# Performance work log

Hardware: AMD Instinct MI355X
Metric: run time of the kernel (lower is better)

The kernel has to match this reference:

```python
import jax, jax.numpy as jnp
import numpy as np

N_EMBD = 1024
N_HEAD = 16
HEAD_DIM = N_EMBD // N_HEAD


def setup_inputs() -> dict:
    key = jax.random.key(0)
    ks = jax.random.split(key, 5)
    B, S = 2, 2048
    scale = 0.02
    return {
        "hidden_states": jax.random.normal(ks[0], (B, S, N_EMBD), dtype=jnp.float32),
        "w_attn": jax.random.normal(ks[1], (N_EMBD, 3 * N_EMBD), dtype=jnp.float32) * scale,
        "b_attn": jnp.zeros((3 * N_EMBD,), dtype=jnp.float32),
        "w_proj": jax.random.normal(ks[2], (N_EMBD, N_EMBD), dtype=jnp.float32) * scale,
        "b_proj": jnp.zeros((N_EMBD,), dtype=jnp.float32),
    }


def reference(hidden_states, w_attn, b_attn, w_proj, b_proj):
    B, S, _ = hidden_states.shape
    qkv = hidden_states @ w_attn + b_attn                     # [B,S,3E]
    q, k, v = jnp.split(qkv, 3, axis=-1)                      # each [B,S,E]

    def split_heads(t):  # [B,S,E] -> [B,H,S,D]
        return t.reshape(B, S, N_HEAD, HEAD_DIM).transpose(0, 2, 1, 3)

    q, k, v = split_heads(q), split_heads(k), split_heads(v)

    scores = jnp.einsum("bhqd,bhkd->bhqk", q, k) / np.sqrt(HEAD_DIM).astype(np.float32)
    causal = jnp.tril(jnp.ones((S, S), dtype=bool))
    scores = jnp.where(causal[None, None], scores, jnp.float32(-jnp.inf))
    attn = jax.nn.softmax(scores, axis=-1)                    # [B,H,S,S]
    out = jnp.einsum("bhqk,bhkd->bhqd", attn, v)              # [B,H,S,D]
    out = out.transpose(0, 2, 1, 3).reshape(B, S, N_EMBD)     # merge heads
    out = out @ w_proj + b_proj
    return out
```

## Files before the change

kernel.cpp:

```cpp
#include <hip/hip_runtime.h>
#include <hip/hip_bf16.h>


typedef __attribute__((ext_vector_type(4))) float  float4v;
typedef __attribute__((ext_vector_type(8))) short  short8v;
typedef __attribute__((ext_vector_type(4))) short  short4v;

#define ATT_SCALE 0.18033688011112042f

__device__ __forceinline__ short f2bf(float f) {
  union { float f; unsigned u; } v; v.f = f;
  unsigned r = v.u + 0x7fffu + ((v.u >> 16) & 1u);
  return (short)(r >> 16);
}
__device__ __forceinline__ float bf2f(short s) {
  union { unsigned u; float f; } v; v.u = ((unsigned)(unsigned short)s) << 16;
  return v.f;
}

__device__ __forceinline__ short4v pack_bf16x4(float a, float b, float c, float d) {
  unsigned x0 = __builtin_bit_cast(unsigned, a) + 0x8000u;
  unsigned x1 = __builtin_bit_cast(unsigned, b) + 0x8000u;
  unsigned x2 = __builtin_bit_cast(unsigned, c) + 0x8000u;
  unsigned x3 = __builtin_bit_cast(unsigned, d) + 0x8000u;
  union { unsigned u[2]; short4v s; } r;
  r.u[0] = __builtin_amdgcn_perm(x1, x0, 0x07060302);
  r.u[1] = __builtin_amdgcn_perm(x3, x2, 0x07060302);
  return r.s;
}

__device__ __forceinline__ void gl_lds16(const void* g, void* l) {
  __builtin_amdgcn_global_load_lds(
      (const __attribute__((address_space(1))) unsigned*)g,
      (__attribute__((address_space(3))) unsigned*)l, 16, 0, 0);
}

__global__ __launch_bounds__(256) void prep_kernel(
    const float* __restrict__ hidden, const float* __restrict__ w_attn,
    const float* __restrict__ w_proj, short* __restrict__ hA,
    short* __restrict__ wqkvT, short* __restrict__ wprojT) {
  __shared__ float tile[32][33];
  const int bx = blockIdx.x, t = threadIdx.x;
  if (bx < 4096) {
    const size_t i = ((size_t)bx * 256 + t) * 4;
    float4v v = *(const float4v*)(hidden + i);
    short4v o;
    #pragma unroll
    for (int k = 0; k < 4; k++) o[k] = f2bf(v[k]);
    *(short4v*)(hA + i) = o;
    return;
  }
  const float* in; short* out; int R, C, cx, cy;
  if (bx < 4096 + 3072) {
    in = w_attn; out = wqkvT; R = 1024; C = 3072;
    cx = (bx - 4096) % 96; cy = (bx - 4096) / 96;
  } else {
    in = w_proj; out = wprojT; R = 1024; C = 1024;
    cx = (bx - 7168) % 32; cy = (bx - 7168) / 32;
  }
  const int tx = t & 31, ty = t >> 5;
  const int c0 = cx * 32, r0 = cy * 32;
  #pragma unroll
  for (int i = 0; i < 4; i++)
    tile[ty + i * 8][tx] = in[(size_t)(r0 + ty + i * 8) * C + c0 + tx];
  __syncthreads();
  #pragma unroll
  for (int i = 0; i < 4; i++) {
    const int cc = ty + i * 8;
    out[(size_t)(c0 + cc) * R + r0 + tx] = f2bf(tile[tx][cc]);
  }
}

template<int RB, int MODE>
__global__ __launch_bounds__(256) void gemm_bt(
    const short* __restrict__ A, const short* __restrict__ Bt,
    const float* __restrict__ bias, void* __restrict__ Cout,
    short* __restrict__ vA, int M, int N, int K)
{
  __shared__ short As[RB][32];
  __shared__ short Bs[128][32];
  const int MI = RB / 32;
  const int t    = threadIdx.x;
  const int lane = t & 63;
  const int wave = t >> 6;
  const int wm   = (wave >> 1) * (RB / 2);
  const int wn   = (wave & 1) * 64;
  const int l16  = lane & 15;
  const int quad = lane >> 4;
  const int row0 = blockIdx.y * RB;
  const int col0 = blockIdx.x * 128;

  float4v acc[MI][4] = {};

  const int srow = lane >> 2;
  const int scol = (lane & 3) * 8;

  for (int k0 = 0; k0 < K; k0 += 32) {
    if (RB == 128) {
      #pragma unroll
      for (int h = 0; h < 2; h++)
        gl_lds16(A + (size_t)(row0 + wave * 32 + h * 16 + srow) * K + k0 + scol,
                 &As[(wave * 32 + h * 16 + srow) & (RB - 1)][scol]);
    } else {
      gl_lds16(A + (size_t)(row0 + wave * 16 + srow) * K + k0 + scol,
               &As[(wave * 16 + srow) & (RB - 1)][scol]);
    }
    #pragma unroll
    for (int h = 0; h < 2; h++)
      gl_lds16(Bt + (size_t)(col0 + wave * 32 + h * 16 + srow) * K + k0 + scol,
               &Bs[wave * 32 + h * 16 + srow][scol]);
    __syncthreads();
    short8v af[MI], bf[4];
    #pragma unroll
    for (int i = 0; i < MI; i++)
      af[i] = *(const short8v*)&As[wm + i * 16 + l16][quad * 8];
    #pragma unroll
    for (int j = 0; j < 4; j++)
      bf[j] = *(const short8v*)&Bs[wn + j * 16 + l16][quad * 8];
    #pragma unroll
    for (int i = 0; i < MI; i++)
      #pragma unroll
      for (int j = 0; j < 4; j++)
        acc[i][j] = __builtin_amdgcn_mfma_f32_16x16x32_bf16(af[i], bf[j], acc[i][j], 0, 0, 0);
    __syncthreads();
  }

  if (MODE == 2 && col0 >= 2048) {
    const int b  = row0 >> 11;
    const int hh = ((col0 - 2048) >> 6) + (wn >> 6);
    const int kt = ((row0 & 2047) >> 6) + (wm >> 6);
    short* vbase = vA + ((size_t)((b * 16 + hh) * 32 + kt) * 8) * 512;
    #pragma unroll
    for (int j = 0; j < 4; j++) {
      const float bv = bias[col0 + wn + j * 16 + l16];
      #pragma unroll
      for (int kwp = 0; kwp < 2; kwp++) {
        short8v s8;
        #pragma unroll
        for (int kw = 0; kw < 2; kw++) {
          short4v q4 = pack_bf16x4(acc[kwp * 2 + kw][j][0] + bv,
                                   acc[kwp * 2 + kw][j][1] + bv,
                                   acc[kwp * 2 + kw][j][2] + bv,
                                   acc[kwp * 2 + kw][j][3] + bv);
          #pragma unroll
          for (int r = 0; r < 4; r++) s8[kw * 4 + r] = q4[r];
        }
        *(short8v*)(vbase + ((size_t)(kwp * 4 + j) * 64 + lane) * 8) = s8;
      }
    }
    return;
  }

  #pragma unroll
  for (int j = 0; j < 4; j++) {
    const int col = col0 + wn + j * 16 + l16;
    const float sc = (MODE == 2 && col < 1024) ? ATT_SCALE : 1.0f;
    const float bv = bias[col];
    #pragma unroll
    for (int i = 0; i < MI; i++) {
      #pragma unroll
      for (int r = 0; r < 4; r++) {
        const int row = row0 + wm + i * 16 + quad * 4 + r;
        const float v = (acc[i][j][r] + bv) * sc;
        if (MODE == 2) ((short*)Cout)[(size_t)row * N + col] = f2bf(v);
        else           ((float*)Cout)[(size_t)row * N + col] = v;
      }
    }
  }
}

__global__ __launch_bounds__(256, 2) void attn_mfma(
    const short* __restrict__ qkv, const short* __restrict__ vA,
    short* __restrict__ P0, short* __restrict__ P1, float* __restrict__ lp)
{
  __shared__ short KA[2][8 * 512];
  __shared__ short VA[2][8 * 512];

  const int bh = blockIdx.y;
  const int b = bh >> 4, h = bh & 15;
  const int s = blockIdx.x;
  int qt = 0, sbase = 0;
  for (;;) { const int nc = (qt >> 3) + 1; if (s < sbase + nc) break; sbase += nc; qt++; }
  const int c = s - sbase;
  const int kt0  = c * 8;
  const int kend = min(qt + 1, kt0 + 8);

  const int t = threadIdx.x;
  const int lane = t & 63, w = t >> 6;
  const int l16 = lane & 15, quad = lane >> 4;

  const size_t base = (size_t)b * 2048 * 3072;
  const int qoff = h * 64, koff = 1024 + h * 64;
  const int qg = qt * 64 + w * 16 + l16;

  short8v qf[2];
  #pragma unroll
  for (int ks = 0; ks < 2; ks++)
    qf[ks] = *(const short8v*)(qkv + base + (size_t)qg * 3072 + qoff + ks * 32 + quad * 8);

  float4v O[4] = {};
  float l = 0.0f;

  const int id0 = w * 2, id1 = id0 + 1;
  const int jm0 = id0 & 3, ks0 = id0 >> 2;
  const int jm1 = id1 & 3, ks1 = id1 >> 2;
  const short* kg0 = qkv + base + (size_t)(jm0 * 16 + l16) * 3072 + koff + ks0 * 32 + quad * 8;
  const short* kg1 = qkv + base + (size_t)(jm1 * 16 + l16) * 3072 + koff + ks1 * 32 + quad * 8;
  const short* vg  = vA + (size_t)(bh * 32) * 4096 + lane * 8;

  gl_lds16(kg0 + (size_t)kt0 * 64 * 3072, &KA[0][id0 * 512 + lane * 8]);
  gl_lds16(kg1 + (size_t)kt0 * 64 * 3072, &KA[0][id1 * 512 + lane * 8]);
  gl_lds16(vg + (size_t)kt0 * 4096 + id0 * 512, &VA[0][id0 * 512 + lane * 8]);
  gl_lds16(vg + (size_t)kt0 * 4096 + id1 * 512, &VA[0][id1 * 512 + lane * 8]);

  for (int kt = kt0; kt < kend; kt++) {
    const int buf = (kt - kt0) & 1;
    __syncthreads();
    if (kt + 1 < kend) {
      gl_lds16(kg0 + (size_t)(kt + 1) * 64 * 3072, &KA[buf ^ 1][id0 * 512 + lane * 8]);
      gl_lds16(kg1 + (size_t)(kt + 1) * 64 * 3072, &KA[buf ^ 1][id1 * 512 + lane * 8]);
      gl_lds16(vg + (size_t)(kt + 1) * 4096 + id0 * 512, &VA[buf ^ 1][id0 * 512 + lane * 8]);
      gl_lds16(vg + (size_t)(kt + 1) * 4096 + id1 * 512, &VA[buf ^ 1][id1 * 512 + lane * 8]);
    }

    float4v sv[4] = {};
    #pragma unroll
    for (int ks = 0; ks < 2; ks++)
      #pragma unroll
      for (int jm = 0; jm < 4; jm++) {
        const short8v kf = *(const short8v*)&KA[buf][(ks * 4 + jm) * 512 + lane * 8];
        sv[jm] = __builtin_amdgcn_mfma_f32_16x16x32_bf16(kf, qf[ks], sv[jm], 0, 0, 0);
      }

    if (kt == qt) {
      #pragma unroll
      for (int jm = 0; jm < 4; jm++) {
        const int kv = kt * 64 + jm * 16 + quad * 4;
        #pragma unroll
        for (int r = 0; r < 4; r++)
          if (kv + r > qg) sv[jm][r] = -INFINITY;
      }
    }

    short4v pk[4];
    #pragma unroll
    for (int jm = 0; jm < 4; jm++) {
      float p0 = exp2f(sv[jm][0]), p1 = exp2f(sv[jm][1]);
      float p2 = exp2f(sv[jm][2]), p3 = exp2f(sv[jm][3]);
      l += (p0 + p1) + (p2 + p3);
      pk[jm] = pack_bf16x4(p0, p1, p2, p3);
    }

    #pragma unroll
    for (int id = 0; id < 8; id++) {
      const int kwp = id >> 2, dm = id & 3;
      const short8v vv = *(const short8v*)&VA[buf][id * 512 + lane * 8];
      const short4v v0 = {vv[0], vv[1], vv[2], vv[3]};
      const short4v v1 = {vv[4], vv[5], vv[6], vv[7]};
      O[dm] = __builtin_amdgcn_mfma_f32_16x16x16bf16_1k(v0, pk[kwp * 2],     O[dm], 0, 0, 0);
      O[dm] = __builtin_amdgcn_mfma_f32_16x16x16bf16_1k(v1, pk[kwp * 2 + 1], O[dm], 0, 0, 0);
    }
  }

  l += __shfl_xor(l, 16);
  l += __shfl_xor(l, 32);
  const int i = bh * 80 + s;
  short* pp = (i < 2048) ? (P0 + (size_t)i * 4096) : (P1 + (size_t)(i - 2048) * 4096);
  const int row = w * 16 + l16;
  if (quad == 0) lp[(size_t)i * 64 + row] = l;
  short* pr = pp + row * 64;
  #pragma unroll
  for (int dm = 0; dm < 4; dm++)
    *(short4v*)(pr + dm * 16 + quad * 4) =
        pack_bf16x4(O[dm][0], O[dm][1], O[dm][2], O[dm][3]);
}

__global__ __launch_bounds__(256) void merge_attn(
    const short* __restrict__ P0, const short* __restrict__ P1,
    const float* __restrict__ lp, short* __restrict__ aout)
{
  const int idx = blockIdx.x * 256 + threadIdx.x;
  const int q = idx >> 7;
  const int rest = idx & 127;
  const int h  = rest >> 3;
  const int dg = (rest & 7) * 8;
  const int b  = q >> 11;
  const int qr = q & 2047;
  const int qt = qr >> 6;
  const int row = qr & 63;
  const int a = qt >> 3, bq = qt & 7;
  const int off = qt + 4 * a * (a - 1) + a * bq;
  const int nc  = a + 1;
  const int bh  = b * 16 + h;

  float acc[8] = {};
  float suml = 0.0f;
  for (int c = 0; c < nc; c++) {
    const int i = bh * 80 + off + c;
    const short* pp = (i < 2048) ? (P0 + (size_t)i * 4096) : (P1 + (size_t)(i - 2048) * 4096);
    const short8v o = *(const short8v*)(pp + row * 64 + dg);
    #pragma unroll
    for (int k = 0; k < 8; k++) acc[k] += bf2f(o[k]);
    suml += lp[(size_t)i * 64 + row];
  }
  const float inv = 1.0f / suml;
  short8v ov;
  #pragma unroll
  for (int k = 0; k < 8; k++) ov[k] = f2bf(acc[k] * inv);
  *(short8v*)(aout + (size_t)q * 1024 + h * 64 + dg) = ov;
}

extern "C" void kernel_launch(void* const* d_in, const int* in_sizes, int n_in,
                              void* d_out, int out_size, void* d_ws, size_t ws_size,
                              hipStream_t stream) {
  const float* hidden = (const float*)d_in[0];
  const float* w_attn = (const float*)d_in[1];
  const float* b_attn = (const float*)d_in[2];
  const float* w_proj = (const float*)d_in[3];
  const float* b_proj = (const float*)d_in[4];
  float* outp = (float*)d_out;

  char* ws = (char*)d_ws;
  short* hA     = (short*)(ws);
  float* lp     = (float*)(ws + 8ull  * 1024 * 1024);
  short* wqkvT  = (short*)(ws + 8ull  * 1024 * 1024);
  short* wprojT = (short*)(ws + 14ull * 1024 * 1024);
  short* qkvb   = (short*)(ws + 16ull * 1024 * 1024);
  short* vAbuf  = (short*)(ws + 40ull * 1024 * 1024);
  short* aout   = (short*)(ws + 40ull * 1024 * 1024);
  short* P0     = (short*)d_out;

  prep_kernel<<<8192, 256, 0, stream>>>(hidden, w_attn, w_proj, hA, wqkvT, wprojT);
  gemm_bt<128, 2><<<dim3(24, 32), 256, 0, stream>>>(hA, wqkvT, b_attn, qkvb, vAbuf, 4096, 3072, 1024);
  attn_mfma<<<dim3(80, 32), 256, 0, stream>>>(qkvb, vAbuf, P0, hA, lp);
  merge_attn<<<2048, 256, 0, stream>>>(P0, hA, lp, aout);
  gemm_bt<64, 0><<<dim3(8, 64), 256, 0, stream>>>(aout, wprojT, b_proj, outp, nullptr, 4096, 1024, 1024);
}
```

Before: 212.8 us.

## Double-buffer GEMM LDS tiles and XOR-swizzle columns to avoid bank conflicts

Turns the bf16 GEMM main loop into a double-buffered pipeline: the next K-slice is issued into the alternate LDS buffer via global-to-LDS loads before the current slice's MFMAs run, and one of the two barriers per iteration is dropped. It also XOR-swizzles the 16-byte column chunk on both the global load side and the LDS read side to reduce bank conflicts. This doubles the LDS footprint per block, which may lower occupancy, and it relies on the single barrier being enough to order buffer reuse.

```diff
diff --git a/kernel.cpp b/kernel.cpp
--- a/kernel.cpp
+++ b/kernel.cpp
@@ -77,8 +77,8 @@
     const float* __restrict__ bias, void* __restrict__ Cout,
     short* __restrict__ vA, int M, int N, int K)
 {
-  __shared__ short As[RB][32];
-  __shared__ short Bs[128][32];
+  __shared__ short As[2][RB][32];
+  __shared__ short Bs[2][128][32];
   const int MI = RB / 32;
   const int t    = threadIdx.x;
   const int lane = t & 63;
@@ -94,35 +94,52 @@
 
   const int srow = lane >> 2;
   const int scol = (lane & 3) * 8;
-
-  for (int k0 = 0; k0 < K; k0 += 32) {
+  const int gcol = ((lane & 3) ^ ((srow >> 1) & 3)) * 8;
+  const int rquad = (quad ^ ((l16 >> 1) & 3)) * 8;
+
+  const short* gA0 = A + (size_t)(row0 + wave * ((RB == 128) ? 32 : 16) + srow) * K + gcol;
+  const short* gA1 = gA0 + (size_t)16 * K;
+  const short* gB0 = Bt + (size_t)(col0 + wave * 32 + srow) * K + gcol;
+  const short* gB1 = gB0 + (size_t)16 * K;
+
+  const int NI = K / 32;
+  {
     if (RB == 128) {
-      #pragma unroll
-      for (int h = 0; h < 2; h++)
-        gl_lds16(A + (size_t)(row0 + wave * 32 + h * 16 + srow) * K + k0 + scol,
-                 &As[(wave * 32 + h * 16 + srow) & (RB - 1)][scol]);
+      gl_lds16(gA0, &As[0][wave * 32 + srow][scol]);
+      gl_lds16(gA1, &As[0][wave * 32 + 16 + srow][scol]);
     } else {
-      gl_lds16(A + (size_t)(row0 + wave * 16 + srow) * K + k0 + scol,
-               &As[(wave * 16 + srow) & (RB - 1)][scol]);
-    }
-    #pragma unroll
-    for (int h = 0; h < 2; h++)
-      gl_lds16(Bt + (size_t)(col0 + wave * 32 + h * 16 + srow) * K + k0 + scol,
-               &Bs[wave * 32 + h * 16 + srow][scol]);
+      gl_lds16(gA0, &As[0][(wave * 16 + srow) & (RB - 1)][scol]);
+    }
+    gl_lds16(gB0, &Bs[0][wave * 32 + srow][scol]);
+    gl_lds16(gB1, &Bs[0][wave * 32 + 16 + srow][scol]);
+  }
+
+  for (int i = 0; i < NI; i++) {
+    const int buf = i & 1;
     __syncthreads();
+    if (i + 1 < NI) {
+      const int k1 = (i + 1) * 32;
+      if (RB == 128) {
+        gl_lds16(gA0 + k1, &As[buf ^ 1][wave * 32 + srow][scol]);
+        gl_lds16(gA1 + k1, &As[buf ^ 1][wave * 32 + 16 + srow][scol]);
+      } else {
+        gl_lds16(gA0 + k1, &As[buf ^ 1][(wave * 16 + srow) & (RB - 1)][scol]);
+      }
+      gl_lds16(gB0 + k1, &Bs[buf ^ 1][wave * 32 + srow][scol]);
+      gl_lds16(gB1 + k1, &Bs[buf ^ 1][wave * 32 + 16 + srow][scol]);
+    }
     short8v af[MI], bf[4];
     #pragma unroll
-    for (int i = 0; i < MI; i++)
-      af[i] = *(const short8v*)&As[wm + i * 16 + l16][quad * 8];
+    for (int ii = 0; ii < MI; ii++)
+      af[ii] = *(const short8v*)&As[buf][wm + ii * 16 + l16][rquad];
     #pragma unroll
     for (int j = 0; j < 4; j++)
-      bf[j] = *(const short8v*)&Bs[wn + j * 16 + l16][quad * 8];
-    #pragma unroll
-    for (int i = 0; i < MI; i++)
+      bf[j] = *(const short8v*)&Bs[buf][wn + j * 16 + l16][rquad];
+    #pragma unroll
+    for (int ii = 0; ii < MI; ii++)
       #pragma unroll
       for (int j = 0; j < 4; j++)
-        acc[i][j] = __builtin_amdgcn_mfma_f32_16x16x32_bf16(af[i], bf[j], acc[i][j], 0, 0, 0);
-    __syncthreads();
+        acc[ii][j] = __builtin_amdgcn_mfma_f32_16x16x32_bf16(af[ii], bf[j], acc[ii][j], 0, 0, 0);
   }
 
   if (MODE == 2 && col0 >= 2048) {
```

Measured after the change: 205.5 us. -3.4%, faster.
